# Kernel optimization log

Measured on AMD Instinct MI355X. Metric: run time of the kernel, lower is better.

## Reference

```python
import jax, jax.numpy as jnp
import numpy as np

IN_DIM = 256
NUM_HEADS = 8
HEAD_DIM = IN_DIM // NUM_HEADS


def setup_inputs() -> dict:
    key = jax.random.key(0)
    k1, k2, k3, k4, k5, k6 = jax.random.split(key, 6)
    B, C, H, W = 2, IN_DIM, 64, 64
    scale = 1.0 / np.sqrt(IN_DIM)
    return {
        "tgt": jax.random.normal(k1, (B, C, H, W), dtype=jnp.float32),
        "src": jax.random.normal(k2, (B, C, H, W), dtype=jnp.float32),
        # nn.Linear weights stored as [out, in] (torch convention); y = x @ W.T
        "Wq": jax.random.normal(k3, (IN_DIM, IN_DIM), dtype=jnp.float32) * scale,
        "Wk": jax.random.normal(k4, (IN_DIM, IN_DIM), dtype=jnp.float32) * scale,
        "Wv": jax.random.normal(k5, (IN_DIM, IN_DIM), dtype=jnp.float32) * scale,
        "Wo": jax.random.normal(k6, (IN_DIM, IN_DIM), dtype=jnp.float32) * scale,
    }


def reference(tgt, src, Wq, Wk, Wv, Wo):
    B, C, H, W = src.shape
    N = H * W
    # b c h w -> b (h w) c
    src_t = src.reshape(B, C, N).transpose(0, 2, 1)
    tgt_t = tgt.reshape(B, C, N).transpose(0, 2, 1)
    # project and split heads: [B, N, C] -> [B, heads, N, head_dim]
    def heads(x, Wt):
        y = jnp.einsum('bnc,dc->bnd', x, Wt)
        return y.reshape(B, N, NUM_HEADS, HEAD_DIM).transpose(0, 2, 1, 3)
    q = heads(tgt_t, Wq)
    k = heads(src_t, Wk)
    v = heads(src_t, Wv)
    scores = jnp.einsum('bhqd,bhkd->bhqk', q, k) / jnp.sqrt(jnp.float32(HEAD_DIM))
    attn = jax.nn.softmax(scores, axis=-1)
    weighted = jnp.einsum('bhqk,bhkd->bhqd', attn, v)  # [B, heads, N, head_dim]
    weighted = weighted.transpose(0, 2, 1, 3).reshape(B, N, C)
    out = jnp.einsum('bnc,dc->bnd', weighted + tgt_t, Wo)
    return out
```

## Files before the change

### kernel.cpp

```cpp
#include <hip/hip_runtime.h>
#include <hip/hip_bf16.h>

#define IN_DIM 256
#define NHEADS 8
#define HDIM 32
#define BATCH 2
#define NTOK 4096
#define QSCALE (0.17677669529663687f * 1.4426950408889634f)

typedef __hip_bfloat16 bf16;
typedef __attribute__((ext_vector_type(8))) short bf16x8;
typedef __attribute__((ext_vector_type(4))) short bf16x4;
typedef __attribute__((ext_vector_type(4))) float f32x4;

union bfrag { bf16x8 v; bf16x4 h[2]; };

__device__ __forceinline__ float b2f(bf16 x) { return __bfloat162float(x); }

#if __has_builtin(__builtin_amdgcn_exp2f)
__device__ __forceinline__ float fast_exp2(float x) { return __builtin_amdgcn_exp2f(x); }
#else
__device__ __forceinline__ float fast_exp2(float x) { return exp2f(x); }
#endif

__device__ __forceinline__ unsigned packbf2(float a, float b) {
    union { __hip_bfloat162 h; unsigned u; } c;
    c.h = __float22bfloat162_rn(float2{a, b});
    return c.u;
}

__device__ __forceinline__ void pack16(float4 a, float4 b, float4 c, float4 d,
                                       bf16* dst) {
    uint2 w0 = {packbf2(a.x, a.y), packbf2(a.z, a.w)};
    uint2 w1 = {packbf2(b.x, b.y), packbf2(b.z, b.w)};
    uint2 w2 = {packbf2(c.x, c.y), packbf2(c.z, c.w)};
    uint2 w3 = {packbf2(d.x, d.y), packbf2(d.z, d.w)};
    *(uint2*)(dst + 0)  = w0;
    *(uint2*)(dst + 4)  = w1;
    *(uint2*)(dst + 8)  = w2;
    *(uint2*)(dst + 12) = w3;
}

__global__ __launch_bounds__(256) void proj_mfma(
    const float* __restrict__ tgt, const float* __restrict__ src,
    const float* __restrict__ Wq, const float* __restrict__ Wk,
    const float* __restrict__ Wv,
    bf16* __restrict__ Qo, bf16* __restrict__ Ko, bf16* __restrict__ Vo)
{
    const int which = blockIdx.y;
    const int dh = blockIdx.z;
    const int b  = blockIdx.x >> 7;
    const int n0 = (blockIdx.x & 127) * 32;
    const float* X = (which == 0) ? tgt : src;
    const float* W = (which == 0) ? Wq : (which == 1 ? Wk : Wv);

    const int tid = threadIdx.x;
    const int wave = tid >> 6, lane = tid & 63;
    const int lg = lane >> 4, lc = lane & 15;
    const int wn = wave & 1, wdq = wave >> 1;

    __shared__ bf16 As[32 * 260];
    __shared__ bf16 Ws[2][128 * 36];

    {
        const float* Xb = X + (size_t)b * IN_DIM * NTOK + n0;
        for (int it = 0; it < 8; ++it) {
            int idx = it * 256 + tid;
            int c = idx >> 3, j4 = idx & 7;
            float4 x = *(const float4*)(Xb + (size_t)c * NTOK + j4 * 4);
            As[(j4 * 4 + 0) * 260 + c] = __float2bfloat16(x.x);
            As[(j4 * 4 + 1) * 260 + c] = __float2bfloat16(x.y);
            As[(j4 * 4 + 2) * 260 + c] = __float2bfloat16(x.z);
            As[(j4 * 4 + 3) * 260 + c] = __float2bfloat16(x.w);
        }
    }
    const int wd = tid >> 1, wc = (tid & 1) * 16;
    const float* Wbase = W + (size_t)(dh * 128 + wd) * IN_DIM + wc;
    {
        float4 a = *(const float4*)(Wbase + 0);
        float4 bb = *(const float4*)(Wbase + 4);
        float4 cc = *(const float4*)(Wbase + 8);
        float4 dd = *(const float4*)(Wbase + 12);
        pack16(a, bb, cc, dd, &Ws[0][wd * 36 + wc]);
    }
    __syncthreads();

    f32x4 acc[4];
    #pragma unroll
    for (int t = 0; t < 4; ++t) acc[t] = f32x4{0.f, 0.f, 0.f, 0.f};

    for (int s = 0; s < 8; ++s) {
        const int c0 = s * 32;
        float4 pa, pb, pc, pd;
        if (s < 7) {
            const float* wn_ = Wbase + (s + 1) * 32;
            pa = *(const float4*)(wn_ + 0);
            pb = *(const float4*)(wn_ + 4);
            pc = *(const float4*)(wn_ + 8);
            pd = *(const float4*)(wn_ + 12);
        }
        bfrag af;
        const bf16* ap = &As[(wn * 16 + lc) * 260 + c0 + lg * 8];
        af.h[0] = *(const bf16x4*)ap;
        af.h[1] = *(const bf16x4*)(ap + 4);
        #pragma unroll
        for (int t = 0; t < 4; ++t) {
            bfrag wf;
            const bf16* wp = &Ws[s & 1][(wdq * 64 + t * 16 + lc) * 36 + lg * 8];
            wf.h[0] = *(const bf16x4*)wp;
            wf.h[1] = *(const bf16x4*)(wp + 4);
            acc[t] = __builtin_amdgcn_mfma_f32_16x16x32_bf16(af.v, wf.v, acc[t], 0, 0, 0);
        }
        if (s < 7) {
            __syncthreads();
            pack16(pa, pb, pc, pd, &Ws[(s + 1) & 1][wd * 36 + wc]);
            __syncthreads();
        }
    }

    const int nb = n0 + wn * 16 + lg * 4;
    if (which == 2) {
        #pragma unroll
        for (int t = 0; t < 4; ++t) {
            int d = dh * 128 + wdq * 64 + t * 16 + lc;
            uint2 pk;
            pk.x = packbf2(acc[t][0], acc[t][1]);
            pk.y = packbf2(acc[t][2], acc[t][3]);
            *(uint2*)(Vo + ((size_t)b * IN_DIM + d) * NTOK + nb) = pk;
        }
    } else {
        const float sc = (which == 0) ? QSCALE : 1.0f;
        bf16* O = (which == 0) ? Qo : Ko;
        #pragma unroll
        for (int t = 0; t < 4; ++t)
            #pragma unroll
            for (int r = 0; r < 4; ++r)
                O[((size_t)b * NTOK + nb + r) * IN_DIM + dh * 128 + wdq * 64 + t * 16 + lc]
                    = __float2bfloat16(acc[t][r] * sc);
    }
}

__global__ __launch_bounds__(256) void attn_mfma_kernel(
    const bf16* __restrict__ Q, const bf16* __restrict__ K,
    const bf16* __restrict__ Vt, const float* __restrict__ tgt,
    bf16* __restrict__ Wt)
{
    const int blk = blockIdx.x;
    const int bh  = 2 * (blk & 7) + ((blk >> 3) & 1);
    const int qb  = blk >> 4;
    const int b = bh >> 3, h = bh & 7;
    const int tid  = threadIdx.x;
    const int wave = tid >> 6;
    const int lane = tid & 63;
    const int lg = lane >> 4, lc = lane & 15;
    const int qw = qb * 128 + wave * 32;

    __shared__ bf16 KL[2][64 * 40];
    __shared__ bf16 VL[2][32 * 72];

    const bf16x8 qfa = *(const bf16x8*)(Q + ((size_t)b * NTOK + qw + lc) * IN_DIM
                                          + h * HDIM + lg * 8);
    const bf16x8 qfb = *(const bf16x8*)(Q + ((size_t)b * NTOK + qw + 16 + lc) * IN_DIM
                                          + h * HDIM + lg * 8);

    bf16x8 ones8;
    #pragma unroll
    for (int i = 0; i < 8; ++i) ((short*)&ones8)[i] = (short)0x3F80;
    const f32x4 z = {0.f, 0.f, 0.f, 0.f};

    const int srow = tid >> 2, sd = (tid & 3) * 8;
    const int vrow = tid >> 3, vch = tid & 7;
    const int kwoff = srow * 40 + sd;
    const int vwoff = vrow * 72 + vch * 8;
    const int kroff = lc * 40 + lg * 8;
    const int vroff0 = lc * 72 + lg * 4;
    const int vroff1 = (16 + lc) * 72 + lg * 4;

    const bf16* Kp = K  + ((size_t)b * NTOK + srow) * IN_DIM + h * HDIM + sd;
    const bf16* Vp = Vt + ((size_t)b * IN_DIM + h * HDIM + vrow) * NTOK + vch * 8;

    f32x4 o0a = {0.f,0.f,0.f,0.f}, o1a = {0.f,0.f,0.f,0.f}, ola = {0.f,0.f,0.f,0.f};
    f32x4 o0b = {0.f,0.f,0.f,0.f}, o1b = {0.f,0.f,0.f,0.f}, olb = {0.f,0.f,0.f,0.f};

    bf16x8 kreg = *(const bf16x8*)Kp;
    bf16x8 vreg = *(const bf16x8*)Vp;
    Kp += (size_t)64 * IN_DIM;
    Vp += 64;

#define HALF(CUR)                                                              \
    {                                                                          \
        *(bf16x8*)&KL[CUR][kwoff] = kreg;                                      \
        *(bf16x8*)&VL[CUR][vwoff] = vreg;                                      \
        kreg = *(const bf16x8*)Kp;                                             \
        vreg = *(const bf16x8*)Vp;                                             \
        Kp += (size_t)64 * IN_DIM;                                             \
        Vp += 64;                                                              \
        __syncthreads();                                                       \
        bf16x8 kf[4];                                                          \
        _Pragma("unroll")                                                      \
        for (int t = 0; t < 4; ++t)                                            \
            kf[t] = *(const bf16x8*)&KL[CUR][kroff + t * 640];                 \
        bf16x4 v0[4], v1[4];                                                   \
        _Pragma("unroll")                                                      \
        for (int t = 0; t < 4; ++t) {                                          \
            v0[t] = *(const bf16x4*)&VL[CUR][vroff0 + t * 16];                 \
            v1[t] = *(const bf16x4*)&VL[CUR][vroff1 + t * 16];                 \
        }                                                                      \
        f32x4 sa[4], sb[4];                                                    \
        __builtin_amdgcn_s_setprio(1);                                         \
        _Pragma("unroll")                                                      \
        for (int t = 0; t < 4; ++t) {                                          \
            sa[t] = __builtin_amdgcn_mfma_f32_16x16x32_bf16(kf[t], qfa, z, 0,0,0); \
            sb[t] = __builtin_amdgcn_mfma_f32_16x16x32_bf16(kf[t], qfb, z, 0,0,0); \
        }                                                                      \
        __builtin_amdgcn_s_setprio(0);                                         \
        _Pragma("unroll")                                                      \
        for (int tcp = 0; tcp < 2; ++tcp) {                                    \
            union { bf16x8 v; uint4 u; } pa, pb;                               \
            pa.u.x = packbf2(fast_exp2(sa[2*tcp][0]),   fast_exp2(sa[2*tcp][1]));   \
            pa.u.y = packbf2(fast_exp2(sa[2*tcp][2]),   fast_exp2(sa[2*tcp][3]));   \
            pa.u.z = packbf2(fast_exp2(sa[2*tcp+1][0]), fast_exp2(sa[2*tcp+1][1])); \
            pa.u.w = packbf2(fast_exp2(sa[2*tcp+1][2]), fast_exp2(sa[2*tcp+1][3])); \
            pb.u.x = packbf2(fast_exp2(sb[2*tcp][0]),   fast_exp2(sb[2*tcp][1]));   \
            pb.u.y = packbf2(fast_exp2(sb[2*tcp][2]),   fast_exp2(sb[2*tcp][3]));   \
            pb.u.z = packbf2(fast_exp2(sb[2*tcp+1][0]), fast_exp2(sb[2*tcp+1][1])); \
            pb.u.w = packbf2(fast_exp2(sb[2*tcp+1][2]), fast_exp2(sb[2*tcp+1][3])); \
            bfrag B0, B1;                                                      \
            B0.h[0] = v0[2*tcp]; B0.h[1] = v0[2*tcp+1];                        \
            B1.h[0] = v1[2*tcp]; B1.h[1] = v1[2*tcp+1];                        \
            __builtin_amdgcn_s_setprio(1);                                     \
            o0a = __builtin_amdgcn_mfma_f32_16x16x32_bf16(pa.v, B0.v, o0a, 0,0,0); \
            o1a = __builtin_amdgcn_mfma_f32_16x16x32_bf16(pa.v, B1.v, o1a, 0,0,0); \
            ola = __builtin_amdgcn_mfma_f32_16x16x32_bf16(pa.v, ones8, ola, 0,0,0); \
            o0b = __builtin_amdgcn_mfma_f32_16x16x32_bf16(pb.v, B0.v, o0b, 0,0,0); \
            o1b = __builtin_amdgcn_mfma_f32_16x16x32_bf16(pb.v, B1.v, o1b, 0,0,0); \
            olb = __builtin_amdgcn_mfma_f32_16x16x32_bf16(pb.v, ones8, olb, 0,0,0); \
            __builtin_amdgcn_s_setprio(0);                                     \
        }                                                                      \
    }

    for (int it = 0; it < NTOK / 128; ++it) {
        HALF(0)
        HALF(1)
    }
#undef HALF

    const float* tga = tgt + ((size_t)b * IN_DIM + h * HDIM + lc) * NTOK + qw + lg * 4;
    float4 r0a = *(const float4*)tga;
    float4 r1a = *(const float4*)(tga + (size_t)16 * NTOK);
    float4 r0b = *(const float4*)(tga + 16);
    float4 r1b = *(const float4*)(tga + (size_t)16 * NTOK + 16);

    bf16* opa = Wt + ((size_t)b * NTOK + qw + lg * 4) * IN_DIM + h * HDIM + lc;
    bf16* opb = opa + (size_t)16 * IN_DIM;
    #pragma unroll
    for (int r = 0; r < 4; ++r) {
        float inva = 1.f / ola[r];
        float invb = 1.f / olb[r];
        opa[(size_t)r * IN_DIM]      = __float2bfloat16(o0a[r] * inva + (&r0a.x)[r]);
        opa[(size_t)r * IN_DIM + 16] = __float2bfloat16(o1a[r] * inva + (&r1a.x)[r]);
        opb[(size_t)r * IN_DIM]      = __float2bfloat16(o0b[r] * invb + (&r0b.x)[r]);
        opb[(size_t)r * IN_DIM + 16] = __float2bfloat16(o1b[r] * invb + (&r1b.x)[r]);
    }
}

__global__ __launch_bounds__(256) void out_mfma(
    const bf16* __restrict__ A, const float* __restrict__ Wo,
    float* __restrict__ out)
{
    const int dh = blockIdx.y;
    const int b  = blockIdx.x >> 7;
    const int n0 = (blockIdx.x & 127) * 32;

    const int tid = threadIdx.x;
    const int wave = tid >> 6, lane = tid & 63;
    const int lg = lane >> 4, lc = lane & 15;
    const int wn = wave & 1, wdq = wave >> 1;

    __shared__ bf16 As[32 * 260];
    __shared__ bf16 Ws[2][128 * 36];

    {
        const bf16* Ab = A + ((size_t)b * NTOK + n0) * IN_DIM;
        for (int it = 0; it < 4; ++it) {
            int idx = it * 256 + tid;
            int r = idx >> 5, ch = idx & 31;
            bfrag v;
            v.v = *(const bf16x8*)(Ab + (size_t)r * IN_DIM + ch * 8);
            *(bf16x4*)&As[r * 260 + ch * 8]     = v.h[0];
            *(bf16x4*)&As[r * 260 + ch * 8 + 4] = v.h[1];
        }
    }
    const int wd = tid >> 1, wc = (tid & 1) * 16;
    const float* Wbase = Wo + (size_t)(dh * 128 + wd) * IN_DIM + wc;
    {
        float4 a = *(const float4*)(Wbase + 0);
        float4 bb = *(const float4*)(Wbase + 4);
        float4 cc = *(const float4*)(Wbase + 8);
        float4 dd = *(const float4*)(Wbase + 12);
        pack16(a, bb, cc, dd, &Ws[0][wd * 36 + wc]);
    }
    __syncthreads();

    f32x4 acc[4];
    #pragma unroll
    for (int t = 0; t < 4; ++t) acc[t] = f32x4{0.f, 0.f, 0.f, 0.f};

    for (int s = 0; s < 8; ++s) {
        const int c0 = s * 32;
        float4 pa, pb, pc, pd;
        if (s < 7) {
            const float* wn_ = Wbase + (s + 1) * 32;
            pa = *(const float4*)(wn_ + 0);
            pb = *(const float4*)(wn_ + 4);
            pc = *(const float4*)(wn_ + 8);
            pd = *(const float4*)(wn_ + 12);
        }
        bfrag af;
        const bf16* ap = &As[(wn * 16 + lc) * 260 + c0 + lg * 8];
        af.h[0] = *(const bf16x4*)ap;
        af.h[1] = *(const bf16x4*)(ap + 4);
        #pragma unroll
        for (int t = 0; t < 4; ++t) {
            bfrag wf;
            const bf16* wp = &Ws[s & 1][(wdq * 64 + t * 16 + lc) * 36 + lg * 8];
            wf.h[0] = *(const bf16x4*)wp;
            wf.h[1] = *(const bf16x4*)(wp + 4);
            acc[t] = __builtin_amdgcn_mfma_f32_16x16x32_bf16(af.v, wf.v, acc[t], 0, 0, 0);
        }
        if (s < 7) {
            __syncthreads();
            pack16(pa, pb, pc, pd, &Ws[(s + 1) & 1][wd * 36 + wc]);
            __syncthreads();
        }
    }

    const int nb = n0 + wn * 16 + lg * 4;
    #pragma unroll
    for (int t = 0; t < 4; ++t)
        #pragma unroll
        for (int r = 0; r < 4; ++r)
            out[((size_t)b * NTOK + nb + r) * IN_DIM + dh * 128 + wdq * 64 + t * 16 + lc]
                = acc[t][r];
}

extern "C" void kernel_launch(void* const* d_in, const int* in_sizes, int n_in,
                              void* d_out, int out_size, void* d_ws, size_t ws_size,
                              hipStream_t stream) {
    const float* tgt = (const float*)d_in[0];
    const float* src = (const float*)d_in[1];
    const float* Wq  = (const float*)d_in[2];
    const float* Wk  = (const float*)d_in[3];
    const float* Wv  = (const float*)d_in[4];
    const float* Wo  = (const float*)d_in[5];
    float* out = (float*)d_out;

    const size_t SZ = (size_t)BATCH * NTOK * IN_DIM * sizeof(bf16);
    char* w = (char*)d_ws;
    bf16* Qb  = (bf16*)(w);
    bf16* Kb  = (bf16*)(w + SZ);
    bf16* Vtb = (bf16*)(w + 2 * SZ);
    bf16* Wt  = (bf16*)(w + 3 * SZ);

    proj_mfma<<<dim3(256, 3, 2), 256, 0, stream>>>(tgt, src, Wq, Wk, Wv, Qb, Kb, Vtb);

    attn_mfma_kernel<<<512, 256, 0, stream>>>(Qb, Kb, Vtb, tgt, Wt);

    out_mfma<<<dim3(256, 2), 256, 0, stream>>>(Wt, Wo, out);
}
```

Before: 97.79 us.

## Split attention key range across two wave groups with LDS reduction

New measurement: 83.54 us. 14.6% less time.

```diff
diff --git a/kernel.cpp b/kernel.cpp
--- a/kernel.cpp
+++ b/kernel.cpp
@@ -140,7 +140,7 @@
     }
 }
 
-__global__ __launch_bounds__(256) void attn_mfma_kernel(
+__global__ __launch_bounds__(512) void attn_mfma_kernel(
     const bf16* __restrict__ Q, const bf16* __restrict__ K,
     const bf16* __restrict__ Vt, const float* __restrict__ tgt,
     bf16* __restrict__ Wt)
@@ -151,12 +151,15 @@
     const int b = bh >> 3, h = bh & 7;
     const int tid  = threadIdx.x;
     const int wave = tid >> 6;
+    const int grp  = wave >> 2;
+    const int wl   = wave & 3;
     const int lane = tid & 63;
     const int lg = lane >> 4, lc = lane & 15;
-    const int qw = qb * 128 + wave * 32;
-
-    __shared__ bf16 KL[2][64 * 40];
-    __shared__ bf16 VL[2][32 * 72];
+    const int qw = qb * 128 + wl * 32;
+
+    __shared__ bf16 KL[2][2][64 * 40];
+    __shared__ bf16 VL[2][2][32 * 72];
+    __shared__ float redC[4][64 * 24];
 
     const bf16x8 qfa = *(const bf16x8*)(Q + ((size_t)b * NTOK + qw + lc) * IN_DIM
                                           + h * HDIM + lg * 8);
@@ -168,16 +171,17 @@
     for (int i = 0; i < 8; ++i) ((short*)&ones8)[i] = (short)0x3F80;
     const f32x4 z = {0.f, 0.f, 0.f, 0.f};
 
-    const int srow = tid >> 2, sd = (tid & 3) * 8;
-    const int vrow = tid >> 3, vch = tid & 7;
+    const int tg   = tid & 255;
+    const int srow = tg >> 2, sd = (tg & 3) * 8;
+    const int vrow = tg >> 3, vch = tg & 7;
     const int kwoff = srow * 40 + sd;
     const int vwoff = vrow * 72 + vch * 8;
     const int kroff = lc * 40 + lg * 8;
     const int vroff0 = lc * 72 + lg * 4;
     const int vroff1 = (16 + lc) * 72 + lg * 4;
 
-    const bf16* Kp = K  + ((size_t)b * NTOK + srow) * IN_DIM + h * HDIM + sd;
-    const bf16* Vp = Vt + ((size_t)b * IN_DIM + h * HDIM + vrow) * NTOK + vch * 8;
+    const bf16* Kp = K  + ((size_t)b * NTOK + grp * 2048 + srow) * IN_DIM + h * HDIM + sd;
+    const bf16* Vp = Vt + ((size_t)b * IN_DIM + h * HDIM + vrow) * NTOK + grp * 2048 + vch * 8;
 
     f32x4 o0a = {0.f,0.f,0.f,0.f}, o1a = {0.f,0.f,0.f,0.f}, ola = {0.f,0.f,0.f,0.f};
     f32x4 o0b = {0.f,0.f,0.f,0.f}, o1b = {0.f,0.f,0.f,0.f}, olb = {0.f,0.f,0.f,0.f};
@@ -189,8 +193,8 @@
 
 #define HALF(CUR)                                                              \
     {                                                                          \
-        *(bf16x8*)&KL[CUR][kwoff] = kreg;                                      \
-        *(bf16x8*)&VL[CUR][vwoff] = vreg;                                      \
+        *(bf16x8*)&KL[grp][CUR][kwoff] = kreg;                                 \
+        *(bf16x8*)&VL[grp][CUR][vwoff] = vreg;                                 \
         kreg = *(const bf16x8*)Kp;                                             \
         vreg = *(const bf16x8*)Vp;                                             \
         Kp += (size_t)64 * IN_DIM;                                             \
@@ -199,12 +203,12 @@
         bf16x8 kf[4];                                                          \
         _Pragma("unroll")                                                      \
         for (int t = 0; t < 4; ++t)                                            \
-            kf[t] = *(const bf16x8*)&KL[CUR][kroff + t * 640];                 \
+            kf[t] = *(const bf16x8*)&KL[grp][CUR][kroff + t * 640];            \
         bf16x4 v0[4], v1[4];                                                   \
         _Pragma("unroll")                                                      \
         for (int t = 0; t < 4; ++t) {                                          \
-            v0[t] = *(const bf16x4*)&VL[CUR][vroff0 + t * 16];                 \
-            v1[t] = *(const bf16x4*)&VL[CUR][vroff1 + t * 16];                 \
+            v0[t] = *(const bf16x4*)&VL[grp][CUR][vroff0 + t * 16];            \
+            v1[t] = *(const bf16x4*)&VL[grp][CUR][vroff1 + t * 16];            \
         }                                                                      \
         f32x4 sa[4], sb[4];                                                    \
         __builtin_amdgcn_s_setprio(1);                                         \
@@ -239,28 +243,44 @@
         }                                                                      \
     }
 
-    for (int it = 0; it < NTOK / 128; ++it) {
+    for (int it = 0; it < NTOK / 256; ++it) {
         HALF(0)
         HALF(1)
     }
 #undef HALF
 
-    const float* tga = tgt + ((size_t)b * IN_DIM + h * HDIM + lc) * NTOK + qw + lg * 4;
-    float4 r0a = *(const float4*)tga;
-    float4 r1a = *(const float4*)(tga + (size_t)16 * NTOK);
-    float4 r0b = *(const float4*)(tga + 16);
-    float4 r1b = *(const float4*)(tga + (size_t)16 * NTOK + 16);
-
-    bf16* opa = Wt + ((size_t)b * NTOK + qw + lg * 4) * IN_DIM + h * HDIM + lc;
-    bf16* opb = opa + (size_t)16 * IN_DIM;
-    #pragma unroll
-    for (int r = 0; r < 4; ++r) {
-        float inva = 1.f / ola[r];
-        float invb = 1.f / olb[r];
-        opa[(size_t)r * IN_DIM]      = __float2bfloat16(o0a[r] * inva + (&r0a.x)[r]);
-        opa[(size_t)r * IN_DIM + 16] = __float2bfloat16(o1a[r] * inva + (&r1a.x)[r]);
-        opb[(size_t)r * IN_DIM]      = __float2bfloat16(o0b[r] * invb + (&r0b.x)[r]);
-        opb[(size_t)r * IN_DIM + 16] = __float2bfloat16(o1b[r] * invb + (&r1b.x)[r]);
+    if (grp) {
+        float* d = &redC[wl][lane * 24];
+        *(f32x4*)(d + 0)  = o0a;  *(f32x4*)(d + 4)  = o1a;  *(f32x4*)(d + 8)  = ola;
+        *(f32x4*)(d + 12) = o0b;  *(f32x4*)(d + 16) = o1b;  *(f32x4*)(d + 20) = olb;
+    }
+    __syncthreads();
+    if (!grp) {
+        const float* s = &redC[wl][lane * 24];
+        o0a += *(const f32x4*)(s + 0);
+        o1a += *(const f32x4*)(s + 4);
+        ola += *(const f32x4*)(s + 8);
+        o0b += *(const f32x4*)(s + 12);
+        o1b += *(const f32x4*)(s + 16);
+        olb += *(const f32x4*)(s + 20);
+
+        const float* tga = tgt + ((size_t)b * IN_DIM + h * HDIM + lc) * NTOK + qw + lg * 4;
+        float4 r0a = *(const float4*)tga;
+        float4 r1a = *(const float4*)(tga + (size_t)16 * NTOK);
+        float4 r0b = *(const float4*)(tga + 16);
+        float4 r1b = *(const float4*)(tga + (size_t)16 * NTOK + 16);
+
+        bf16* opa = Wt + ((size_t)b * NTOK + qw + lg * 4) * IN_DIM + h * HDIM + lc;
+        bf16* opb = opa + (size_t)16 * IN_DIM;
+        #pragma unroll
+        for (int r = 0; r < 4; ++r) {
+            float inva = 1.f / ola[r];
+            float invb = 1.f / olb[r];
+            opa[(size_t)r * IN_DIM]      = __float2bfloat16(o0a[r] * inva + (&r0a.x)[r]);
+            opa[(size_t)r * IN_DIM + 16] = __float2bfloat16(o1a[r] * inva + (&r1a.x)[r]);
+            opb[(size_t)r * IN_DIM]      = __float2bfloat16(o0b[r] * invb + (&r0b.x)[r]);
+            opb[(size_t)r * IN_DIM + 16] = __float2bfloat16(o1b[r] * invb + (&r1b.x)[r]);
+        }
     }
 }
 
@@ -364,7 +384,7 @@
 
     proj_mfma<<<dim3(256, 3, 2), 256, 0, stream>>>(tgt, src, Wq, Wk, Wv, Qb, Kb, Vtb);
 
-    attn_mfma_kernel<<<512, 256, 0, stream>>>(Qb, Kb, Vtb, tgt, Wt);
+    attn_mfma_kernel<<<512, 512, 0, stream>>>(Qb, Kb, Vtb, tgt, Wt);
 
     out_mfma<<<dim3(256, 2), 256, 0, stream>>>(Wt, Wo, out);
 }
```
